# Performance work log

Hardware: AMD Instinct MI355X
Metric: run time of the kernel (lower is better)

The kernel has to match this reference:

```python
import jax, jax.numpy as jnp
import numpy as np

N = 50000
E = 800000
F_IN = 128
HID = 128
OUT = 64
EPS = 1e-5


def gcn_conv(x, src, dst, deg_inv_sqrt, W, b):
    # h = x @ W  (dense transform first, like PyG GCNConv)
    h = x @ W  # [N, F_out]
    norm = deg_inv_sqrt[src] * deg_inv_sqrt[dst]  # [E+N] (self-loops included)
    msgs = norm[:, None] * h[src]  # gather + scale, [E+N, F_out]
    out = jax.ops.segment_sum(msgs, dst, num_segments=N)  # scatter-add to targets
    return out + b


def setup_inputs() -> dict:
    key = jax.random.key(0)
    ks = jax.random.split(key, 9)
    x = jax.random.normal(ks[0], (N, F_IN), dtype=jnp.float32)
    edge_index = jax.random.randint(ks[1], (2, E), 0, N, dtype=jnp.int64)
    s = 1.0 / np.sqrt(F_IN)
    W1 = jax.random.uniform(ks[2], (F_IN, HID), jnp.float32, -s, s)
    b1 = jnp.zeros((HID,), jnp.float32)
    sh = 1.0 / np.sqrt(HID)
    Wmu = jax.random.uniform(ks[3], (HID, OUT), jnp.float32, -sh, sh)
    bmu = jnp.zeros((OUT,), jnp.float32)
    Wlv = jax.random.uniform(ks[4], (HID, OUT), jnp.float32, -sh, sh)
    blv = jnp.zeros((OUT,), jnp.float32)
    gamma = jnp.ones((HID,), jnp.float32)
    beta = jnp.zeros((HID,), jnp.float32)
    return {"x": x, "edge_index": edge_index, "W1": W1, "b1": b1,
            "gamma": gamma, "beta": beta, "Wmu": Wmu, "bmu": bmu,
            "Wlv": Wlv, "blv": blv}


def reference(x, edge_index, W1, b1, gamma, beta, Wmu, bmu, Wlv, blv):
    # Add self-loops (GCNConv default) and compute symmetric normalization once.
    loop = jnp.arange(N, dtype=edge_index.dtype)
    src = jnp.concatenate([edge_index[0], loop])
    dst = jnp.concatenate([edge_index[1], loop])
    deg = jax.ops.segment_sum(jnp.ones_like(dst, dtype=x.dtype), dst, num_segments=N)
    deg_inv_sqrt = jnp.where(deg > 0, jax.lax.rsqrt(deg), 0.0)

    h = jax.nn.relu(gcn_conv(x, src, dst, deg_inv_sqrt, W1, b1))
    # per-node LayerNorm over feature dim
    mean = jnp.mean(h, axis=-1, keepdims=True)
    var = jnp.var(h, axis=-1, keepdims=True)
    h = (h - mean) * jax.lax.rsqrt(var + EPS) * gamma + beta

    mu = gcn_conv(h, src, dst, deg_inv_sqrt, Wmu, bmu)
    logvar = gcn_conv(h, src, dst, deg_inv_sqrt, Wlv, blv)
    return mu, logvar
```

## Files before the change

### kernel.cpp

```cpp
#include <hip/hip_runtime.h>

#define NN 50000
#define EE 800000
#define FF 128
#define OO 64
#define EPSF 1e-5f
#define SCB 196
#define EBLK 3125
#define GBLK 391
#define NB 256
#define EPB 3125
#define NW 12500

typedef unsigned int uint;
typedef unsigned short ushort;
typedef unsigned char uchar;
typedef __attribute__((ext_vector_type(8))) short short8;
typedef __attribute__((ext_vector_type(4))) float f32x4;
typedef __attribute__((ext_vector_type(4))) float floatx4;

__device__ __forceinline__ float bflo(uint v) { return __uint_as_float(v << 16); }
__device__ __forceinline__ float bfhi(uint v) { return __uint_as_float(v & 0xFFFF0000u); }
__device__ __forceinline__ uint f2bf(float f) {
  uint b = __float_as_uint(f);
  return (b + 0x7FFFu + ((b >> 16) & 1u)) >> 16;
}
__device__ __forceinline__ uint pack2(float x, float y) { return f2bf(x) | (f2bf(y) << 16); }

__device__ __forceinline__ int eidx(const void* ei, long long pos, int f64) {
  if (f64) return (int)((const long long*)ei)[pos];
  return ((const int*)ei)[pos];
}

__device__ __forceinline__ int detect_f64(const void* ei) {
  int lane = threadIdx.x & 63;
  int probe = ((const int*)ei)[2 * lane + 1];
  return __any(probe != 0) ? 0 : 1;
}

__global__ __launch_bounds__(512) void k_hist(const void* ei,
                                              uint* __restrict__ histW,
                                              uchar* __restrict__ lrank) {
  __shared__ uint lh[NW];
  for (int w = threadIdx.x; w < NW; w += 512) lh[w] = 0;
  __syncthreads();
  int f64 = detect_f64(ei);
  int b = blockIdx.x;
  for (int i = threadIdx.x; i < EPB; i += 512) {
    int e = b * EPB + i;
    int d = eidx(ei, (long long)EE + e, f64);
    int sh = (d & 3) * 8;
    uint old = atomicAdd(&lh[d >> 2], 1u << sh);
    lrank[e] = (uchar)((old >> sh) & 255u);
  }
  __syncthreads();
  uint* dst = histW + (size_t)b * NW;
  for (int w = threadIdx.x; w < NW; w += 512) dst[w] = lh[w];
}

__global__ __launch_bounds__(256) void k_boff(const uint* __restrict__ histW,
                                              uint* __restrict__ boffW,
                                              int* __restrict__ cnt) {
  int w = blockIdx.x * 256 + threadIdx.x;
  if (w >= NW) return;
  uint s0 = 0, s1 = 0, s2 = 0, s3 = 0;
  for (int b = 0; b < NB; ++b) {
    uint hv = histW[(size_t)b * NW + w];
    boffW[(size_t)b * NW + w] = s0 | (s1 << 8) | (s2 << 16) | (s3 << 24);
    s0 += hv & 255u; s1 += (hv >> 8) & 255u;
    s2 += (hv >> 16) & 255u; s3 += (hv >> 24) & 255u;
  }
  int4 c4;
  c4.x = (int)s0; c4.y = (int)s1; c4.z = (int)s2; c4.w = (int)s3;
  ((int4*)cnt)[w] = c4;
}

__global__ __launch_bounds__(512) void k_grank(const void* ei,
                                               const uint* __restrict__ boffW,
                                               const uchar* __restrict__ lrank,
                                               int* __restrict__ grank) {
  __shared__ uint sb[NW];
  int b = blockIdx.x;
  const uint* src = boffW + (size_t)b * NW;
  for (int w = threadIdx.x; w < NW; w += 512) sb[w] = src[w];
  __syncthreads();
  int f64 = detect_f64(ei);
  int e0 = b * EPB;
  for (int i = threadIdx.x; i < EPB; i += 512) {
    int e = e0 + i;
    int d = eidx(ei, (long long)EE + e, f64);
    uint bw = sb[d >> 2];
    grank[e] = (int)((bw >> ((d & 3) * 8)) & 255u) + (int)lrank[e];
  }
}

__global__ __launch_bounds__(256) void k_dis_part(const int* __restrict__ cnt,
                                                  float* __restrict__ dis,
                                                  int* __restrict__ bsum) {
  int i = blockIdx.x * 256 + threadIdx.x;
  int v = (i < NN) ? cnt[i] : 0;
  if (i < NN) dis[i] = rsqrtf((float)(v + 1));
  int s = v;
#pragma unroll
  for (int m = 1; m < 64; m <<= 1) s += __shfl_xor(s, m);
  __shared__ int ws[4];
  if ((threadIdx.x & 63) == 0) ws[threadIdx.x >> 6] = s;
  __syncthreads();
  if (threadIdx.x == 0) bsum[blockIdx.x] = ws[0] + ws[1] + ws[2] + ws[3];
}

__global__ __launch_bounds__(256) void k_scan_all(const int* __restrict__ cnt,
                                                  const int* __restrict__ bsum,
                                                  int* __restrict__ rowptr) {
  __shared__ int s[256];
  __shared__ int vv[256];
  __shared__ int wsum[4];
  int tid = threadIdx.x, blk = blockIdx.x;
  int v = (tid < SCB) ? bsum[tid] : 0;
  s[tid] = v;
  vv[tid] = v;
  __syncthreads();
  for (int off = 1; off < 256; off <<= 1) {
    int t = (tid >= off) ? s[tid - off] : 0;
    __syncthreads();
    s[tid] += t;
    __syncthreads();
  }
  if (blk == 0 && tid == 255) rowptr[NN] = s[255];
  int boff = s[blk] - vv[blk];
  int i = blk * 256 + tid;
  int c = (i < NN) ? cnt[i] : 0;
  int lane = tid & 63, wid = tid >> 6;
  int inc = c;
#pragma unroll
  for (int off = 1; off < 64; off <<= 1) {
    int t = __shfl_up(inc, off);
    if (lane >= off) inc += t;
  }
  if (lane == 63) wsum[wid] = inc;
  __syncthreads();
  int wadd = 0;
  for (int wj = 0; wj < wid; ++wj) wadd += wsum[wj];
  int exc = inc - c + wadd + boff;
  if (i < NN) rowptr[i] = exc;
}

__device__ __forceinline__ int wt_idx(int c, int k) {
  return c * 128 + (k ^ ((c & 7) << 3));
}

__global__ __launch_bounds__(256) void k_scatter_gemm1(
    const void* ei, const float* __restrict__ dis,
    const int* __restrict__ rowptr, const int* __restrict__ grank,
    int2* __restrict__ cw,
    const float* __restrict__ X, const float* __restrict__ W,
    ushort* __restrict__ T) {
  __shared__ ushort Wt[FF * FF];
  if (blockIdx.x >= GBLK) {
    int e = (blockIdx.x - GBLK) * 256 + threadIdx.x;
    if (e >= EE) return;
    int f64 = detect_f64(ei);
    int s = eidx(ei, e, f64);
    int d = eidx(ei, (long long)EE + e, f64);
    int p = rowptr[d] + grank[e];
    int2 v;
    v.x = s;
    v.y = __float_as_int(dis[s] * dis[d]);
    cw[p] = v;
    return;
  }
  for (int i = threadIdx.x; i < FF * FF; i += 256) {
    int k = i >> 7, c = i & 127;
    Wt[wt_idx(c, k)] = (ushort)f2bf(W[i]);
  }
  __syncthreads();
  int l = threadIdx.x & 63, wv = threadIdx.x >> 6;
  int rbase = blockIdx.x * 128 + wv * 32;
  int lr = l & 15, lk = (l >> 4) << 3;
  f32x4 acc[2][8] = {};
#pragma unroll
  for (int kb = 0; kb < 4; ++kb) {
    int kk = kb * 32 + lk;
    short8 a[2];
#pragma unroll
    for (int rt = 0; rt < 2; ++rt) {
      int row = min(rbase + rt * 16 + lr, NN - 1);
      const float4* ap = (const float4*)(X + (size_t)row * FF + kk);
      float4 x0 = ap[0], x1 = ap[1];
      a[rt][0] = (short)f2bf(x0.x); a[rt][1] = (short)f2bf(x0.y);
      a[rt][2] = (short)f2bf(x0.z); a[rt][3] = (short)f2bf(x0.w);
      a[rt][4] = (short)f2bf(x1.x); a[rt][5] = (short)f2bf(x1.y);
      a[rt][6] = (short)f2bf(x1.z); a[rt][7] = (short)f2bf(x1.w);
    }
#pragma unroll
    for (int ct = 0; ct < 8; ++ct) {
      int c = ct * 16 + lr;
      short8 b = *(const short8*)&Wt[wt_idx(c, kk)];
      acc[0][ct] = __builtin_amdgcn_mfma_f32_16x16x32_bf16(a[0], b, acc[0][ct], 0, 0, 0);
      acc[1][ct] = __builtin_amdgcn_mfma_f32_16x16x32_bf16(a[1], b, acc[1][ct], 0, 0, 0);
    }
  }
  int rl = (l >> 4) * 4;
#pragma unroll
  for (int rt = 0; rt < 2; ++rt)
#pragma unroll
    for (int reg = 0; reg < 4; ++reg) {
      int row = rbase + rt * 16 + rl + reg;
      if (row < NN) {
#pragma unroll
        for (int ct = 0; ct < 8; ++ct)
          T[(size_t)row * FF + ct * 16 + lr] = (ushort)f2bf(acc[rt][ct][reg]);
      }
    }
}

__global__ __launch_bounds__(256) void k_gemmHW(const ushort* __restrict__ A,
                                                const float* __restrict__ Wmu,
                                                const float* __restrict__ Wlv,
                                                ushort* __restrict__ T) {
  __shared__ ushort Wt[FF * FF];
  for (int i = threadIdx.x; i < FF * FF; i += 256) {
    int k = i >> 7, c = i & 127;
    float v = (c < OO) ? Wmu[k * OO + c] : Wlv[k * OO + (c - OO)];
    Wt[wt_idx(c, k)] = (ushort)f2bf(v);
  }
  __syncthreads();
  int l = threadIdx.x & 63, wv = threadIdx.x >> 6;
  int rbase = blockIdx.x * 128 + wv * 32;
  int lr = l & 15, lk = (l >> 4) << 3;
  f32x4 acc[2][8] = {};
#pragma unroll
  for (int kb = 0; kb < 4; ++kb) {
    int kk = kb * 32 + lk;
    short8 a[2];
#pragma unroll
    for (int rt = 0; rt < 2; ++rt) {
      int row = min(rbase + rt * 16 + lr, NN - 1);
      a[rt] = *(const short8*)(A + (size_t)row * FF + kk);
    }
#pragma unroll
    for (int ct = 0; ct < 8; ++ct) {
      int c = ct * 16 + lr;
      short8 b = *(const short8*)&Wt[wt_idx(c, kk)];
      acc[0][ct] = __builtin_amdgcn_mfma_f32_16x16x32_bf16(a[0], b, acc[0][ct], 0, 0, 0);
      acc[1][ct] = __builtin_amdgcn_mfma_f32_16x16x32_bf16(a[1], b, acc[1][ct], 0, 0, 0);
    }
  }
  int rl = (l >> 4) * 4;
#pragma unroll
  for (int rt = 0; rt < 2; ++rt)
#pragma unroll
    for (int reg = 0; reg < 4; ++reg) {
      int row = rbase + rt * 16 + rl + reg;
      if (row < NN) {
#pragma unroll
        for (int ct = 0; ct < 8; ++ct)
          T[(size_t)row * FF + ct * 16 + lr] = (ushort)f2bf(acc[rt][ct][reg]);
      }
    }
}

__global__ __launch_bounds__(256) void k_gather_ln(const int* __restrict__ rowptr,
                                                   const int2* __restrict__ cw,
                                                   const float* __restrict__ dis,
                                                   const ushort* __restrict__ feat,
                                                   const float* __restrict__ b1,
                                                   const float* __restrict__ gamma,
                                                   const float* __restrict__ beta,
                                                   ushort* __restrict__ outp) {
  int node = blockIdx.x * 4 + (threadIdx.x >> 6);
  if (node >= NN) return;
  int l = threadIdx.x & 63;
  int g = l >> 4;
  int c16 = l & 15;

  float di = dis[node];
  uint4 vSelf = ((const uint4*)(feat + ((size_t)node << 7)))[c16];

  float acc[8] = {};
  int e0 = rowptr[node], nE = rowptr[node + 1] - e0;
  int base = 0;
  for (; base + 8 <= nE; base += 8) {
    int2 cA = cw[e0 + base + g];
    int2 cB = cw[e0 + base + 4 + g];
    uint4 vA = ((const uint4*)(feat + ((size_t)cA.x << 7)))[c16];
    uint4 vB = ((const uint4*)(feat + ((size_t)cB.x << 7)))[c16];
    float wA = __int_as_float(cA.y), wB = __int_as_float(cB.y);
    acc[0] = fmaf(wA, bflo(vA.x), acc[0]); acc[1] = fmaf(wA, bfhi(vA.x), acc[1]);
    acc[2] = fmaf(wA, bflo(vA.y), acc[2]); acc[3] = fmaf(wA, bfhi(vA.y), acc[3]);
    acc[4] = fmaf(wA, bflo(vA.z), acc[4]); acc[5] = fmaf(wA, bfhi(vA.z), acc[5]);
    acc[6] = fmaf(wA, bflo(vA.w), acc[6]); acc[7] = fmaf(wA, bfhi(vA.w), acc[7]);
    acc[0] = fmaf(wB, bflo(vB.x), acc[0]); acc[1] = fmaf(wB, bfhi(vB.x), acc[1]);
    acc[2] = fmaf(wB, bflo(vB.y), acc[2]); acc[3] = fmaf(wB, bfhi(vB.y), acc[3]);
    acc[4] = fmaf(wB, bflo(vB.z), acc[4]); acc[5] = fmaf(wB, bfhi(vB.z), acc[5]);
    acc[6] = fmaf(wB, bflo(vB.w), acc[6]); acc[7] = fmaf(wB, bfhi(vB.w), acc[7]);
  }
#pragma unroll
  for (int t = 0; t < 2; ++t) {
    int idx = base + t * 4 + g;
    if (idx < nE) {
      int2 c0 = cw[e0 + idx];
      uint4 v = ((const uint4*)(feat + ((size_t)c0.x << 7)))[c16];
      float w0 = __int_as_float(c0.y);
      acc[0] = fmaf(w0, bflo(v.x), acc[0]); acc[1] = fmaf(w0, bfhi(v.x), acc[1]);
      acc[2] = fmaf(w0, bflo(v.y), acc[2]); acc[3] = fmaf(w0, bfhi(v.y), acc[3]);
      acc[4] = fmaf(w0, bflo(v.z), acc[4]); acc[5] = fmaf(w0, bfhi(v.z), acc[5]);
      acc[6] = fmaf(w0, bflo(v.w), acc[6]); acc[7] = fmaf(w0, bfhi(v.w), acc[7]);
    }
  }
#pragma unroll
  for (int j = 0; j < 8; ++j) {
    acc[j] += __shfl_xor(acc[j], 16);
    acc[j] += __shfl_xor(acc[j], 32);
  }
  {
    float sw = di * di;
    acc[0] = fmaf(sw, bflo(vSelf.x), acc[0]); acc[1] = fmaf(sw, bfhi(vSelf.x), acc[1]);
    acc[2] = fmaf(sw, bflo(vSelf.y), acc[2]); acc[3] = fmaf(sw, bfhi(vSelf.y), acc[3]);
    acc[4] = fmaf(sw, bflo(vSelf.z), acc[4]); acc[5] = fmaf(sw, bfhi(vSelf.z), acc[5]);
    acc[6] = fmaf(sw, bflo(vSelf.w), acc[6]); acc[7] = fmaf(sw, bfhi(vSelf.w), acc[7]);
  }
  int cOff = c16 * 8;
  float4 ba = *(const float4*)&b1[cOff];
  float4 bb = *(const float4*)&b1[cOff + 4];
  float a[8];
  a[0] = fmaxf(acc[0] + ba.x, 0.f); a[1] = fmaxf(acc[1] + ba.y, 0.f);
  a[2] = fmaxf(acc[2] + ba.z, 0.f); a[3] = fmaxf(acc[3] + ba.w, 0.f);
  a[4] = fmaxf(acc[4] + bb.x, 0.f); a[5] = fmaxf(acc[5] + bb.y, 0.f);
  a[6] = fmaxf(acc[6] + bb.z, 0.f); a[7] = fmaxf(acc[7] + bb.w, 0.f);
  float s = 0.f, sq = 0.f;
#pragma unroll
  for (int j = 0; j < 8; ++j) { s += a[j]; sq += a[j] * a[j]; }
#pragma unroll
  for (int m = 1; m < 16; m <<= 1) {
    s += __shfl_xor(s, m);
    sq += __shfl_xor(sq, m);
  }
  float mean = s * (1.f / 128.f);
  float var = sq * (1.f / 128.f) - mean * mean;
  float rstd = rsqrtf(var + EPSF);
  float4 ga = *(const float4*)&gamma[cOff];
  float4 gb = *(const float4*)&gamma[cOff + 4];
  float4 ea = *(const float4*)&beta[cOff];
  float4 eb = *(const float4*)&beta[cOff + 4];
  float o[8];
  o[0] = (a[0] - mean) * rstd * ga.x + ea.x; o[1] = (a[1] - mean) * rstd * ga.y + ea.y;
  o[2] = (a[2] - mean) * rstd * ga.z + ea.z; o[3] = (a[3] - mean) * rstd * ga.w + ea.w;
  o[4] = (a[4] - mean) * rstd * gb.x + eb.x; o[5] = (a[5] - mean) * rstd * gb.y + eb.y;
  o[6] = (a[6] - mean) * rstd * gb.z + eb.z; o[7] = (a[7] - mean) * rstd * gb.w + eb.w;
  if (g == 0) {
    uint4 p;
    p.x = pack2(o[0], o[1]); p.y = pack2(o[2], o[3]);
    p.z = pack2(o[4], o[5]); p.w = pack2(o[6], o[7]);
    ((uint4*)(outp + ((size_t)node << 7)))[c16] = p;
  }
}

__global__ __launch_bounds__(256) void k_gather_out(const int* __restrict__ rowptr,
                                                    const int2* __restrict__ cw,
                                                    const float* __restrict__ dis,
                                                    const ushort* __restrict__ feat,
                                                    const float* __restrict__ bmu,
                                                    const float* __restrict__ blv,
                                                    float* __restrict__ out) {
  int node = blockIdx.x * 4 + (threadIdx.x >> 6);
  if (node >= NN) return;
  int l = threadIdx.x & 63;
  int g = l >> 4;
  int c16 = l & 15;

  float di = dis[node];
  uint4 vSelf = ((const uint4*)(feat + ((size_t)node << 7)))[c16];

  float acc[8] = {};
  int e0 = rowptr[node], nE = rowptr[node + 1] - e0;
  int base = 0;
  for (; base + 8 <= nE; base += 8) {
    int2 cA = cw[e0 + base + g];
    int2 cB = cw[e0 + base + 4 + g];
    uint4 vA = ((const uint4*)(feat + ((size_t)cA.x << 7)))[c16];
    uint4 vB = ((const uint4*)(feat + ((size_t)cB.x << 7)))[c16];
    float wA = __int_as_float(cA.y), wB = __int_as_float(cB.y);
    acc[0] = fmaf(wA, bflo(vA.x), acc[0]); acc[1] = fmaf(wA, bfhi(vA.x), acc[1]);
    acc[2] = fmaf(wA, bflo(vA.y), acc[2]); acc[3] = fmaf(wA, bfhi(vA.y), acc[3]);
    acc[4] = fmaf(wA, bflo(vA.z), acc[4]); acc[5] = fmaf(wA, bfhi(vA.z), acc[5]);
    acc[6] = fmaf(wA, bflo(vA.w), acc[6]); acc[7] = fmaf(wA, bfhi(vA.w), acc[7]);
    acc[0] = fmaf(wB, bflo(vB.x), acc[0]); acc[1] = fmaf(wB, bfhi(vB.x), acc[1]);
    acc[2] = fmaf(wB, bflo(vB.y), acc[2]); acc[3] = fmaf(wB, bfhi(vB.y), acc[3]);
    acc[4] = fmaf(wB, bflo(vB.z), acc[4]); acc[5] = fmaf(wB, bfhi(vB.z), acc[5]);
    acc[6] = fmaf(wB, bflo(vB.w), acc[6]); acc[7] = fmaf(wB, bfhi(vB.w), acc[7]);
  }
#pragma unroll
  for (int t = 0; t < 2; ++t) {
    int idx = base + t * 4 + g;
    if (idx < nE) {
      int2 c0 = cw[e0 + idx];
      uint4 v = ((const uint4*)(feat + ((size_t)c0.x << 7)))[c16];
      float w0 = __int_as_float(c0.y);
      acc[0] = fmaf(w0, bflo(v.x), acc[0]); acc[1] = fmaf(w0, bfhi(v.x), acc[1]);
      acc[2] = fmaf(w0, bflo(v.y), acc[2]); acc[3] = fmaf(w0, bfhi(v.y), acc[3]);
      acc[4] = fmaf(w0, bflo(v.z), acc[4]); acc[5] = fmaf(w0, bfhi(v.z), acc[5]);
      acc[6] = fmaf(w0, bflo(v.w), acc[6]); acc[7] = fmaf(w0, bfhi(v.w), acc[7]);
    }
  }
#pragma unroll
  for (int j = 0; j < 8; ++j) {
    acc[j] += __shfl_xor(acc[j], 16);
    acc[j] += __shfl_xor(acc[j], 32);
  }
  {
    float sw = di * di;
    acc[0] = fmaf(sw, bflo(vSelf.x), acc[0]); acc[1] = fmaf(sw, bfhi(vSelf.x), acc[1]);
    acc[2] = fmaf(sw, bflo(vSelf.y), acc[2]); acc[3] = fmaf(sw, bfhi(vSelf.y), acc[3]);
    acc[4] = fmaf(sw, bflo(vSelf.z), acc[4]); acc[5] = fmaf(sw, bfhi(vSelf.z), acc[5]);
    acc[6] = fmaf(sw, bflo(vSelf.w), acc[6]); acc[7] = fmaf(sw, bfhi(vSelf.w), acc[7]);
  }
  if (g == 0) {
    const float* bsrc = (c16 < 8) ? (bmu + c16 * 8) : (blv + (c16 - 8) * 8);
    float* osrc = (c16 < 8) ? (out + (size_t)node * OO + c16 * 8)
                            : (out + (size_t)NN * OO + (size_t)node * OO + (c16 - 8) * 8);
    float4 b0 = *(const float4*)bsrc;
    float4 b1 = *(const float4*)(bsrc + 4);
    floatx4 o0 = { acc[0] + b0.x, acc[1] + b0.y, acc[2] + b0.z, acc[3] + b0.w };
    floatx4 o1 = { acc[4] + b1.x, acc[5] + b1.y, acc[6] + b1.z, acc[7] + b1.w };
    __builtin_nontemporal_store(o0, (floatx4*)osrc);
    __builtin_nontemporal_store(o1, (floatx4*)(osrc + 4));
  }
}

extern "C" void kernel_launch(void* const* d_in, const int* in_sizes, int n_in,
                              void* d_out, int out_size, void* d_ws, size_t ws_size,
                              hipStream_t stream) {
  const float* x     = (const float*)d_in[0];
  const void*  ei    = d_in[1];
  const float* W1    = (const float*)d_in[2];
  const float* b1    = (const float*)d_in[3];
  const float* gamma = (const float*)d_in[4];
  const float* beta  = (const float*)d_in[5];
  const float* Wmu   = (const float*)d_in[6];
  const float* bmu   = (const float*)d_in[7];
  const float* Wlv   = (const float*)d_in[8];
  const float* blv   = (const float*)d_in[9];
  float* out = (float*)d_out;

  int*   rowptr = (int*)d_ws;
  float* dis    = (float*)(rowptr + (NN + 16));
  int*   bsum   = (int*)(dis + NN);
  int*   cnt    = bsum + 256;
  uint*  histW  = (uint*)(cnt + NN);
  uint*  boffW  = histW + (size_t)NB * NW;
  uchar* lrank  = (uchar*)(boffW + (size_t)NB * NW);
  int*   grank  = (int*)(lrank + EE);
  size_t off32  = (size_t)(NN + 16) + NN + 256 + NN + 2 * (size_t)NB * NW + EE / 4 + EE;
  off32 = (off32 + 63) & ~(size_t)63;
  int2*  cw     = (int2*)((int*)d_ws + off32);
  ushort* t  = (ushort*)(cw + EE);
  ushort* h  = t + (size_t)NN * FF;
  ushort* hw = h + (size_t)NN * FF;

  k_hist<<<NB, 512, 0, stream>>>(ei, histW, lrank);
  k_boff<<<(NW + 255) / 256, 256, 0, stream>>>(histW, boffW, cnt);
  k_grank<<<NB, 512, 0, stream>>>(ei, boffW, lrank, grank);
  k_dis_part<<<SCB, 256, 0, stream>>>(cnt, dis, bsum);
  k_scan_all<<<SCB, 256, 0, stream>>>(cnt, bsum, rowptr);
  k_scatter_gemm1<<<GBLK + EBLK, 256, 0, stream>>>(ei, dis, rowptr, grank, cw, x, W1, t);

  k_gather_ln<<<(NN + 3) / 4, 256, 0, stream>>>(rowptr, cw, dis, t, b1, gamma, beta, h);
  k_gemmHW<<<GBLK, 256, 0, stream>>>(h, Wmu, Wlv, hw);
  k_gather_out<<<(NN + 3) / 4, 256, 0, stream>>>(rowptr, cw, dis, hw, bmu, blv, out);
}
```

Before: 153.7 us.

## Fold dis/bsum into k_boff and overlap CSR scatter with gather-LN halves

The degree rsqrt and per-block sums move into k_boff, which removes the k_dis_part launch. The edge scatter into CSR is split by destination node: edges for the first half of the nodes are scattered alongside GEMM1, and edges for the second half are scattered in a kernel that also runs gather+LayerNorm for the first half. A final kernel handles gather+LN for the second half. The aim is to overlap scatter work with gather work and cut launches. In exchange, each edge's destination index is read twice and the edge blocks partially idle.

```diff
diff --git a/kernel.cpp b/kernel.cpp
--- a/kernel.cpp
+++ b/kernel.cpp
@@ -6,11 +6,13 @@
 #define OO 64
 #define EPSF 1e-5f
 #define SCB 196
-#define EBLK 3125
 #define GBLK 391
 #define NB 256
 #define EPB 3125
 #define NW 12500
+#define EBLK 3125
+#define NSPLIT 25000
+#define GA_BLK 6250
 
 typedef unsigned int uint;
 typedef unsigned short ushort;
@@ -60,53 +62,30 @@
 
 __global__ __launch_bounds__(256) void k_boff(const uint* __restrict__ histW,
                                               uint* __restrict__ boffW,
-                                              int* __restrict__ cnt) {
+                                              int* __restrict__ cnt,
+                                              float* __restrict__ dis,
+                                              int* __restrict__ bsum) {
   int w = blockIdx.x * 256 + threadIdx.x;
-  if (w >= NW) return;
   uint s0 = 0, s1 = 0, s2 = 0, s3 = 0;
-  for (int b = 0; b < NB; ++b) {
-    uint hv = histW[(size_t)b * NW + w];
-    boffW[(size_t)b * NW + w] = s0 | (s1 << 8) | (s2 << 16) | (s3 << 24);
-    s0 += hv & 255u; s1 += (hv >> 8) & 255u;
-    s2 += (hv >> 16) & 255u; s3 += (hv >> 24) & 255u;
-  }
-  int4 c4;
-  c4.x = (int)s0; c4.y = (int)s1; c4.z = (int)s2; c4.w = (int)s3;
-  ((int4*)cnt)[w] = c4;
-}
-
-__global__ __launch_bounds__(512) void k_grank(const void* ei,
-                                               const uint* __restrict__ boffW,
-                                               const uchar* __restrict__ lrank,
-                                               int* __restrict__ grank) {
-  __shared__ uint sb[NW];
-  int b = blockIdx.x;
-  const uint* src = boffW + (size_t)b * NW;
-  for (int w = threadIdx.x; w < NW; w += 512) sb[w] = src[w];
-  __syncthreads();
-  int f64 = detect_f64(ei);
-  int e0 = b * EPB;
-  for (int i = threadIdx.x; i < EPB; i += 512) {
-    int e = e0 + i;
-    int d = eidx(ei, (long long)EE + e, f64);
-    uint bw = sb[d >> 2];
-    grank[e] = (int)((bw >> ((d & 3) * 8)) & 255u) + (int)lrank[e];
-  }
-}
-
-__global__ __launch_bounds__(256) void k_dis_part(const int* __restrict__ cnt,
-                                                  float* __restrict__ dis,
-                                                  int* __restrict__ bsum) {
-  int i = blockIdx.x * 256 + threadIdx.x;
-  int v = (i < NN) ? cnt[i] : 0;
-  if (i < NN) dis[i] = rsqrtf((float)(v + 1));
-  int s = v;
-#pragma unroll
-  for (int m = 1; m < 64; m <<= 1) s += __shfl_xor(s, m);
-  __shared__ int ws[4];
-  if ((threadIdx.x & 63) == 0) ws[threadIdx.x >> 6] = s;
-  __syncthreads();
-  if (threadIdx.x == 0) bsum[blockIdx.x] = ws[0] + ws[1] + ws[2] + ws[3];
+  if (w < NW) {
+    for (int b = 0; b < NB; ++b) {
+      uint hv = histW[(size_t)b * NW + w];
+      boffW[(size_t)b * NW + w] = s0 | (s1 << 8) | (s2 << 16) | (s3 << 24);
+      s0 += hv & 255u; s1 += (hv >> 8) & 255u;
+      s2 += (hv >> 16) & 255u; s3 += (hv >> 24) & 255u;
+    }
+    int4 c4;
+    c4.x = (int)s0; c4.y = (int)s1; c4.z = (int)s2; c4.w = (int)s3;
+    ((int4*)cnt)[w] = c4;
+    float4 d4;
+    d4.x = rsqrtf((float)(s0 + 1)); d4.y = rsqrtf((float)(s1 + 1));
+    d4.z = rsqrtf((float)(s2 + 1)); d4.w = rsqrtf((float)(s3 + 1));
+    ((float4*)dis)[w] = d4;
+  }
+  int ss = (int)(s0 + s1 + s2 + s3);
+#pragma unroll
+  for (int m = 1; m < 64; m <<= 1) ss += __shfl_xor(ss, m);
+  if ((threadIdx.x & 63) == 0) bsum[blockIdx.x * 4 + (threadIdx.x >> 6)] = ss;
 }
 
 __global__ __launch_bounds__(256) void k_scan_all(const int* __restrict__ cnt,
@@ -145,138 +124,38 @@
   if (i < NN) rowptr[i] = exc;
 }
 
+__global__ __launch_bounds__(512) void k_grank(const void* ei,
+                                               const uint* __restrict__ boffW,
+                                               const uchar* __restrict__ lrank,
+                                               int* __restrict__ grank) {
+  __shared__ uint sb[NW];
+  int b = blockIdx.x;
+  const uint* src = boffW + (size_t)b * NW;
+  for (int w = threadIdx.x; w < NW; w += 512) sb[w] = src[w];
+  __syncthreads();
+  int f64 = detect_f64(ei);
+  int e0 = b * EPB;
+  for (int i = threadIdx.x; i < EPB; i += 512) {
+    int e = e0 + i;
+    int d = eidx(ei, (long long)EE + e, f64);
+    uint bw = sb[d >> 2];
+    grank[e] = (int)((bw >> ((d & 3) * 8)) & 255u) + (int)lrank[e];
+  }
+}
+
 __device__ __forceinline__ int wt_idx(int c, int k) {
   return c * 128 + (k ^ ((c & 7) << 3));
 }
 
-__global__ __launch_bounds__(256) void k_scatter_gemm1(
-    const void* ei, const float* __restrict__ dis,
-    const int* __restrict__ rowptr, const int* __restrict__ grank,
-    int2* __restrict__ cw,
-    const float* __restrict__ X, const float* __restrict__ W,
-    ushort* __restrict__ T) {
-  __shared__ ushort Wt[FF * FF];
-  if (blockIdx.x >= GBLK) {
-    int e = (blockIdx.x - GBLK) * 256 + threadIdx.x;
-    if (e >= EE) return;
-    int f64 = detect_f64(ei);
-    int s = eidx(ei, e, f64);
-    int d = eidx(ei, (long long)EE + e, f64);
-    int p = rowptr[d] + grank[e];
-    int2 v;
-    v.x = s;
-    v.y = __float_as_int(dis[s] * dis[d]);
-    cw[p] = v;
-    return;
-  }
-  for (int i = threadIdx.x; i < FF * FF; i += 256) {
-    int k = i >> 7, c = i & 127;
-    Wt[wt_idx(c, k)] = (ushort)f2bf(W[i]);
-  }
-  __syncthreads();
-  int l = threadIdx.x & 63, wv = threadIdx.x >> 6;
-  int rbase = blockIdx.x * 128 + wv * 32;
-  int lr = l & 15, lk = (l >> 4) << 3;
-  f32x4 acc[2][8] = {};
-#pragma unroll
-  for (int kb = 0; kb < 4; ++kb) {
-    int kk = kb * 32 + lk;
-    short8 a[2];
-#pragma unroll
-    for (int rt = 0; rt < 2; ++rt) {
-      int row = min(rbase + rt * 16 + lr, NN - 1);
-      const float4* ap = (const float4*)(X + (size_t)row * FF + kk);
-      float4 x0 = ap[0], x1 = ap[1];
-      a[rt][0] = (short)f2bf(x0.x); a[rt][1] = (short)f2bf(x0.y);
-      a[rt][2] = (short)f2bf(x0.z); a[rt][3] = (short)f2bf(x0.w);
-      a[rt][4] = (short)f2bf(x1.x); a[rt][5] = (short)f2bf(x1.y);
-      a[rt][6] = (short)f2bf(x1.z); a[rt][7] = (short)f2bf(x1.w);
-    }
-#pragma unroll
-    for (int ct = 0; ct < 8; ++ct) {
-      int c = ct * 16 + lr;
-      short8 b = *(const short8*)&Wt[wt_idx(c, kk)];
-      acc[0][ct] = __builtin_amdgcn_mfma_f32_16x16x32_bf16(a[0], b, acc[0][ct], 0, 0, 0);
-      acc[1][ct] = __builtin_amdgcn_mfma_f32_16x16x32_bf16(a[1], b, acc[1][ct], 0, 0, 0);
-    }
-  }
-  int rl = (l >> 4) * 4;
-#pragma unroll
-  for (int rt = 0; rt < 2; ++rt)
-#pragma unroll
-    for (int reg = 0; reg < 4; ++reg) {
-      int row = rbase + rt * 16 + rl + reg;
-      if (row < NN) {
-#pragma unroll
-        for (int ct = 0; ct < 8; ++ct)
-          T[(size_t)row * FF + ct * 16 + lr] = (ushort)f2bf(acc[rt][ct][reg]);
-      }
-    }
-}
-
-__global__ __launch_bounds__(256) void k_gemmHW(const ushort* __restrict__ A,
-                                                const float* __restrict__ Wmu,
-                                                const float* __restrict__ Wlv,
-                                                ushort* __restrict__ T) {
-  __shared__ ushort Wt[FF * FF];
-  for (int i = threadIdx.x; i < FF * FF; i += 256) {
-    int k = i >> 7, c = i & 127;
-    float v = (c < OO) ? Wmu[k * OO + c] : Wlv[k * OO + (c - OO)];
-    Wt[wt_idx(c, k)] = (ushort)f2bf(v);
-  }
-  __syncthreads();
-  int l = threadIdx.x & 63, wv = threadIdx.x >> 6;
-  int rbase = blockIdx.x * 128 + wv * 32;
-  int lr = l & 15, lk = (l >> 4) << 3;
-  f32x4 acc[2][8] = {};
-#pragma unroll
-  for (int kb = 0; kb < 4; ++kb) {
-    int kk = kb * 32 + lk;
-    short8 a[2];
-#pragma unroll
-    for (int rt = 0; rt < 2; ++rt) {
-      int row = min(rbase + rt * 16 + lr, NN - 1);
-      a[rt] = *(const short8*)(A + (size_t)row * FF + kk);
-    }
-#pragma unroll
-    for (int ct = 0; ct < 8; ++ct) {
-      int c = ct * 16 + lr;
-      short8 b = *(const short8*)&Wt[wt_idx(c, kk)];
-      acc[0][ct] = __builtin_amdgcn_mfma_f32_16x16x32_bf16(a[0], b, acc[0][ct], 0, 0, 0);
-      acc[1][ct] = __builtin_amdgcn_mfma_f32_16x16x32_bf16(a[1], b, acc[1][ct], 0, 0, 0);
-    }
-  }
-  int rl = (l >> 4) * 4;
-#pragma unroll
-  for (int rt = 0; rt < 2; ++rt)
-#pragma unroll
-    for (int reg = 0; reg < 4; ++reg) {
-      int row = rbase + rt * 16 + rl + reg;
-      if (row < NN) {
-#pragma unroll
-        for (int ct = 0; ct < 8; ++ct)
-          T[(size_t)row * FF + ct * 16 + lr] = (ushort)f2bf(acc[rt][ct][reg]);
-      }
-    }
-}
-
-__global__ __launch_bounds__(256) void k_gather_ln(const int* __restrict__ rowptr,
-                                                   const int2* __restrict__ cw,
-                                                   const float* __restrict__ dis,
-                                                   const ushort* __restrict__ feat,
-                                                   const float* __restrict__ b1,
-                                                   const float* __restrict__ gamma,
-                                                   const float* __restrict__ beta,
-                                                   ushort* __restrict__ outp) {
-  int node = blockIdx.x * 4 + (threadIdx.x >> 6);
-  if (node >= NN) return;
-  int l = threadIdx.x & 63;
+__device__ __forceinline__ void gather_ln_node(
+    int node, int l, const int* __restrict__ rowptr, const int2* __restrict__ cw,
+    const float* __restrict__ dis, const ushort* __restrict__ feat,
+    const float* __restrict__ b1, const float* __restrict__ gamma,
+    const float* __restrict__ beta, ushort* __restrict__ outp) {
   int g = l >> 4;
   int c16 = l & 15;
-
   float di = dis[node];
   uint4 vSelf = ((const uint4*)(feat + ((size_t)node << 7)))[c16];
-
   float acc[8] = {};
   int e0 = rowptr[node], nE = rowptr[node + 1] - e0;
   int base = 0;
@@ -356,6 +235,154 @@
   }
 }
 
+__global__ __launch_bounds__(256) void k_scatter_gemm1(
+    const void* ei, const float* __restrict__ dis,
+    const int* __restrict__ rowptr, const int* __restrict__ grank,
+    int2* __restrict__ cw,
+    const float* __restrict__ X, const float* __restrict__ W,
+    ushort* __restrict__ T) {
+  __shared__ ushort Wt[FF * FF];
+  if (blockIdx.x >= GBLK) {
+    int e = (blockIdx.x - GBLK) * 256 + threadIdx.x;
+    if (e >= EE) return;
+    int f64 = detect_f64(ei);
+    int d = eidx(ei, (long long)EE + e, f64);
+    if (d >= NSPLIT) return;
+    int s = eidx(ei, e, f64);
+    int p = rowptr[d] + grank[e];
+    int2 v;
+    v.x = s;
+    v.y = __float_as_int(dis[s] * dis[d]);
+    cw[p] = v;
+    return;
+  }
+  for (int i = threadIdx.x; i < FF * FF; i += 256) {
+    int k = i >> 7, c = i & 127;
+    Wt[wt_idx(c, k)] = (ushort)f2bf(W[i]);
+  }
+  __syncthreads();
+  int l = threadIdx.x & 63, wv = threadIdx.x >> 6;
+  int rbase = blockIdx.x * 128 + wv * 32;
+  int lr = l & 15, lk = (l >> 4) << 3;
+  f32x4 acc[2][8] = {};
+#pragma unroll
+  for (int kb = 0; kb < 4; ++kb) {
+    int kk = kb * 32 + lk;
+    short8 a[2];
+#pragma unroll
+    for (int rt = 0; rt < 2; ++rt) {
+      int row = min(rbase + rt * 16 + lr, NN - 1);
+      const float4* ap = (const float4*)(X + (size_t)row * FF + kk);
+      float4 x0 = ap[0], x1 = ap[1];
+      a[rt][0] = (short)f2bf(x0.x); a[rt][1] = (short)f2bf(x0.y);
+      a[rt][2] = (short)f2bf(x0.z); a[rt][3] = (short)f2bf(x0.w);
+      a[rt][4] = (short)f2bf(x1.x); a[rt][5] = (short)f2bf(x1.y);
+      a[rt][6] = (short)f2bf(x1.z); a[rt][7] = (short)f2bf(x1.w);
+    }
+#pragma unroll
+    for (int ct = 0; ct < 8; ++ct) {
+      int c = ct * 16 + lr;
+      short8 b = *(const short8*)&Wt[wt_idx(c, kk)];
+      acc[0][ct] = __builtin_amdgcn_mfma_f32_16x16x32_bf16(a[0], b, acc[0][ct], 0, 0, 0);
+      acc[1][ct] = __builtin_amdgcn_mfma_f32_16x16x32_bf16(a[1], b, acc[1][ct], 0, 0, 0);
+    }
+  }
+  int rl = (l >> 4) * 4;
+#pragma unroll
+  for (int rt = 0; rt < 2; ++rt)
+#pragma unroll
+    for (int reg = 0; reg < 4; ++reg) {
+      int row = rbase + rt * 16 + rl + reg;
+      if (row < NN) {
+#pragma unroll
+        for (int ct = 0; ct < 8; ++ct)
+          T[(size_t)row * FF + ct * 16 + lr] = (ushort)f2bf(acc[rt][ct][reg]);
+      }
+    }
+}
+
+__global__ __launch_bounds__(256) void k_scatB_gA(
+    const void* ei, const float* __restrict__ dis,
+    const int* __restrict__ rowptr, const int* __restrict__ grank,
+    int2* __restrict__ cw,
+    const ushort* __restrict__ feat, const float* __restrict__ b1,
+    const float* __restrict__ gamma, const float* __restrict__ beta,
+    ushort* __restrict__ outp) {
+  if (blockIdx.x < EBLK) {
+    int e = blockIdx.x * 256 + threadIdx.x;
+    if (e >= EE) return;
+    int f64 = detect_f64(ei);
+    int d = eidx(ei, (long long)EE + e, f64);
+    if (d < NSPLIT) return;
+    int s = eidx(ei, e, f64);
+    int p = rowptr[d] + grank[e];
+    int2 v;
+    v.x = s;
+    v.y = __float_as_int(dis[s] * dis[d]);
+    cw[p] = v;
+    return;
+  }
+  int node = (blockIdx.x - EBLK) * 4 + (threadIdx.x >> 6);
+  if (node >= NSPLIT) return;
+  gather_ln_node(node, threadIdx.x & 63, rowptr, cw, dis, feat, b1, gamma, beta, outp);
+}
+
+__global__ __launch_bounds__(256) void k_gather_lnB(
+    const int* __restrict__ rowptr, const int2* __restrict__ cw,
+    const float* __restrict__ dis, const ushort* __restrict__ feat,
+    const float* __restrict__ b1, const float* __restrict__ gamma,
+    const float* __restrict__ beta, ushort* __restrict__ outp) {
+  int node = NSPLIT + blockIdx.x * 4 + (threadIdx.x >> 6);
+  if (node >= NN) return;
+  gather_ln_node(node, threadIdx.x & 63, rowptr, cw, dis, feat, b1, gamma, beta, outp);
+}
+
+__global__ __launch_bounds__(256) void k_gemmHW(const ushort* __restrict__ A,
+                                                const float* __restrict__ Wmu,
+                                                const float* __restrict__ Wlv,
+                                                ushort* __restrict__ T) {
+  __shared__ ushort Wt[FF * FF];
+  for (int i = threadIdx.x; i < FF * FF; i += 256) {
+    int k = i >> 7, c = i & 127;
+    float v = (c < OO) ? Wmu[k * OO + c] : Wlv[k * OO + (c - OO)];
+    Wt[wt_idx(c, k)] = (ushort)f2bf(v);
+  }
+  __syncthreads();
+  int l = threadIdx.x & 63, wv = threadIdx.x >> 6;
+  int rbase = blockIdx.x * 128 + wv * 32;
+  int lr = l & 15, lk = (l >> 4) << 3;
+  f32x4 acc[2][8] = {};
+#pragma unroll
+  for (int kb = 0; kb < 4; ++kb) {
+    int kk = kb * 32 + lk;
+    short8 a[2];
+#pragma unroll
+    for (int rt = 0; rt < 2; ++rt) {
+      int row = min(rbase + rt * 16 + lr, NN - 1);
+      a[rt] = *(const short8*)(A + (size_t)row * FF + kk);
+    }
+#pragma unroll
+    for (int ct = 0; ct < 8; ++ct) {
+      int c = ct * 16 + lr;
+      short8 b = *(const short8*)&Wt[wt_idx(c, kk)];
+      acc[0][ct] = __builtin_amdgcn_mfma_f32_16x16x32_bf16(a[0], b, acc[0][ct], 0, 0, 0);
+      acc[1][ct] = __builtin_amdgcn_mfma_f32_16x16x32_bf16(a[1], b, acc[1][ct], 0, 0, 0);
+    }
+  }
+  int rl = (l >> 4) * 4;
+#pragma unroll
+  for (int rt = 0; rt < 2; ++rt)
+#pragma unroll
+    for (int reg = 0; reg < 4; ++reg) {
+      int row = rbase + rt * 16 + rl + reg;
+      if (row < NN) {
+#pragma unroll
+        for (int ct = 0; ct < 8; ++ct)
+          T[(size_t)row * FF + ct * 16 + lr] = (ushort)f2bf(acc[rt][ct][reg]);
+      }
+    }
+}
+
 __global__ __launch_bounds__(256) void k_gather_out(const int* __restrict__ rowptr,
                                                     const int2* __restrict__ cw,
                                                     const float* __restrict__ dis,
@@ -459,13 +486,14 @@
   ushort* hw = h + (size_t)NN * FF;
 
   k_hist<<<NB, 512, 0, stream>>>(ei, histW, lrank);
-  k_boff<<<(NW + 255) / 256, 256, 0, stream>>>(histW, boffW, cnt);
+  k_boff<<<(NW + 255) / 256, 256, 0, stream>>>(histW, boffW, cnt, dis, bsum);
+  k_scan_all<<<SCB, 256, 0, stream>>>(cnt, bsum, rowptr);
   k_grank<<<NB, 512, 0, stream>>>(ei, boffW, lrank, grank);
-  k_dis_part<<<SCB, 256, 0, stream>>>(cnt, dis, bsum);
-  k_scan_all<<<SCB, 256, 0, stream>>>(cnt, bsum, rowptr);
+
   k_scatter_gemm1<<<GBLK + EBLK, 256, 0, stream>>>(ei, dis, rowptr, grank, cw, x, W1, t);
-
-  k_gather_ln<<<(NN + 3) / 4, 256, 0, stream>>>(rowptr, cw, dis, t, b1, gamma, beta, h);
+  k_scatB_gA<<<EBLK + GA_BLK, 256, 0, stream>>>(ei, dis, rowptr, grank, cw,
+                                                t, b1, gamma, beta, h);
+  k_gather_lnB<<<GA_BLK, 256, 0, stream>>>(rowptr, cw, dis, t, b1, gamma, beta, h);
   k_gemmHW<<<GBLK, 256, 0, stream>>>(h, Wmu, Wlv, hw);
   k_gather_out<<<(NN + 3) / 4, 256, 0, stream>>>(rowptr, cw, dis, hw, bmu, blv, out);
 }
```

New measurement: 161.0 us. 4.8% more time.
